# Optimization experiments

Measured on AMD Instinct MI355X. Metric: run time of the kernel, lower is better.

## Reference

```python
import jax, jax.numpy as jnp
import numpy as np

K_SIZE = 3
CH_IN = 256
NFILT = 256

def setup_inputs() -> dict:
    key = jax.random.key(0)
    k1, k2 = jax.random.split(key)
    x = jax.random.normal(k1, (32, 56, 56, CH_IN), dtype=jnp.float32)
    stdv = 1.0 / np.sqrt(K_SIZE * K_SIZE * CH_IN)
    w = jax.random.normal(k2, (K_SIZE, K_SIZE, CH_IN, NFILT), dtype=jnp.float32) * stdv
    pruning_mask = jnp.ones((K_SIZE * K_SIZE * CH_IN, NFILT), dtype=jnp.float32)
    return {"x": x, "w": w, "pruning_mask": pruning_mask}

def _magnitude_aware_weight(w):
    # scale = mean |w| over (kh, kw, cin), per output filter; stop-gradient
    scale = jax.lax.stop_gradient(jnp.mean(jnp.abs(w), axis=(0, 1, 2), keepdims=True))
    bw_no_grad = scale * jnp.sign(w)
    clipped = jnp.clip(w, -1.0, 1.0)
    # STE: forward = scale*sign(w), backward = d(clip(w,-1,1))
    return jax.lax.stop_gradient(bw_no_grad) - jax.lax.stop_gradient(clipped) + clipped

def reference(x, w, pruning_mask):
    kernel = _magnitude_aware_weight(w) * pruning_mask.reshape(K_SIZE, K_SIZE, CH_IN, NFILT)
    out = jax.lax.conv_general_dilated(
        x, kernel,
        window_strides=(1, 1),
        padding="SAME",
        dimension_numbers=("NHWC", "HWIO", "NHWC"),
    )
    return out
```

## Files before the change

### kernel.cpp

```cpp
#include <hip/hip_runtime.h>

typedef unsigned short u16;
typedef u16 u16x8 __attribute__((ext_vector_type(8)));
typedef __bf16 bf16x8 __attribute__((ext_vector_type(8)));
typedef float f32x4 __attribute__((ext_vector_type(4)));

#define NPIX 100352
#define KTOT 2304
#define IMG_PAD (58 * 58 * 256)

static __device__ __forceinline__ u16 f2bf(float f) {
  unsigned u = __float_as_uint(f);
  return (u16)((u + 0x7fffu + ((u >> 16) & 1u)) >> 16);
}

static __device__ __forceinline__ void gld_lds16(const u16* g, u16* l) {
  __builtin_amdgcn_global_load_lds(
      (const __attribute__((address_space(1))) void*)g,
      (__attribute__((address_space(3))) void*)l, 16, 0, 0);
}

static __device__ __forceinline__ int ka_of(int kt) {
  const int khw = kt >> 2;
  const int q = (khw * 11) >> 5;
  const int r = khw - q * 3;
  return (q * 58 + r - 59) * 256 + (kt & 3) * 64;
}

__global__ void scale_accum_k(const float* __restrict__ w, float* __restrict__ scale) {
  const int t = threadIdx.x;
  const float* p = w + (long)blockIdx.x * 64 * 256 + t;
  float acc = 0.f;
#pragma unroll
  for (int e = 0; e < 64; ++e) acc += fabsf(p[(long)e * 256]);
  atomicAdd(&scale[t], acc);
}

__global__ void pack_w_k(const float* __restrict__ w, const float* __restrict__ mask,
                         const float* __restrict__ ssum, u16* __restrict__ wp) {
  __shared__ u16 t[128][33];
  const int k0 = blockIdx.x * 32;
  const int f0 = blockIdx.y * 128;
  const int tid = threadIdx.x;
#pragma unroll
  for (int i = 0; i < 16; ++i) {
    int idx = tid + i * 256;
    int kk = idx >> 7;
    int ff = idx & 127;
    long g = (long)(k0 + kk) * 256 + f0 + ff;
    float wv = w[g];
    float mv = mask[g];
    float sc = ssum[f0 + ff] * (1.0f / 2304.0f);
    float sg = (wv > 0.f) ? 1.f : ((wv < 0.f) ? -1.f : 0.f);
    t[ff][kk] = f2bf(sc * sg * mv);
  }
  __syncthreads();
#pragma unroll
  for (int i = 0; i < 8; ++i) {
    int idx = tid + i * 256;
    int row = idx >> 4;
    int c = idx & 15;
    unsigned v = (unsigned)t[row][2 * c] | ((unsigned)t[row][2 * c + 1] << 16);
    *(unsigned*)(wp + (long)(f0 + row) * KTOT + k0 + 2 * c) = v;
  }
}

__global__ __launch_bounds__(256) void fill_xpad3_k(const float* __restrict__ x,
                                                    u16* __restrict__ xp) {
  const int img = blockIdx.y;
  const int ph = blockIdx.x;
  u16* rowp = xp + ((img * 58 + ph) * 58) * 256;
  const bool irow = (ph >= 1 && ph <= 56);
  const float* xrow = x + ((long)img * 3136 + (ph - 1) * 56) * 256;
  for (int i = threadIdx.x; i < 58 * 32; i += 256) {
    const int pw = i >> 5;
    const int c8 = (i & 31) * 8;
    u16x8 v = {0, 0, 0, 0, 0, 0, 0, 0};
    if (irow && pw >= 1 && pw <= 56) {
      const float* s = xrow + (pw - 1) * 256 + c8;
      float4 a = *(const float4*)s;
      float4 b = *(const float4*)(s + 4);
      v[0] = f2bf(a.x); v[1] = f2bf(a.y); v[2] = f2bf(a.z); v[3] = f2bf(a.w);
      v[4] = f2bf(b.x); v[5] = f2bf(b.y); v[6] = f2bf(b.z); v[7] = f2bf(b.w);
    }
    *(u16x8*)(rowp + pw * 256 + c8) = v;
  }
}

#define STAGE_A8(kt, h, b) do { const int _ka = ka_of(kt); \
    gld_lds16(aptr[(h)*2]     + _ka, As[b] + ldso[(h)*2]); \
    gld_lds16(aptr[(h)*2 + 1] + _ka, As[b] + ldso[(h)*2 + 1]); } while (0)
#define STAGE_B8(kt, h, b) do { const int _kb = (kt) * 64; \
    gld_lds16(bptr[(h)*2]     + _kb, Bs[b] + ldso[(h)*2]); \
    gld_lds16(bptr[(h)*2 + 1] + _kb, Bs[b] + ldso[(h)*2 + 1]); } while (0)

__global__ __launch_bounds__(512, 2) void conv_gemm8_k(
    const u16* __restrict__ xpad, const u16* __restrict__ wp, float* __restrict__ out) {
  __shared__ u16 As[2][256 * 64];
  __shared__ u16 Bs[2][256 * 64];

  const int tid = threadIdx.x;
  const int lane = tid & 63;
  const int wid = tid >> 6;

  const int orig = blockIdx.x;
  const int swz = (orig & 7) * 49 + (orig >> 3);
  const int m0 = swz * 256;

  const int lsub = lane >> 3;
  const int lc = (lane & 7) ^ lsub;
  const u16* aptr[4];
  const u16* bptr[4];
  int ldso[4];
#pragma unroll
  for (int q = 0; q < 4; ++q) {
    const int o = (q >> 1) * 16 + (q & 1) * 8 + wid;
    const int row = o * 8 + lsub;
    const int m = m0 + row;
    const int img = m / 3136, pix = m % 3136;
    aptr[q] = xpad + (long)img * IMG_PAD + ((pix / 56 + 1) * 58 + (pix % 56) + 1) * 256 + lc * 8;
    bptr[q] = wp + (long)row * KTOT + lc * 8;
    ldso[q] = o * 512;
  }

  const int lm = lane & 15, kq = lane >> 4;
  const int wm = wid >> 2, wn = wid & 3;
  int pcq[2];
  pcq[0] = (kq ^ (lm & 7)) * 8;
  pcq[1] = ((4 + kq) ^ (lm & 7)) * 8;
  const int aB = (wm * 128 + lm) * 64;
  const int bB = (wn * 64 + lm) * 64;

  f32x4 acc[8][4] = {};
  bf16x8 bv[4][2];

  STAGE_B8(0, 0, 0); STAGE_B8(0, 1, 0);
  STAGE_A8(0, 0, 0); STAGE_A8(0, 1, 0);
  STAGE_B8(1, 0, 1); STAGE_B8(1, 1, 1);
  asm volatile("s_waitcnt vmcnt(4)" ::: "memory");
  __builtin_amdgcn_s_barrier();
  asm volatile("" ::: "memory");

  for (int J = 0; J < 17; ++J) {
#pragma unroll
    for (int p = 0; p < 8; ++p) {
      const int buf = p >> 2;
      const int pp = p & 3;
      if (pp == 0) {
#pragma unroll
        for (int ni = 0; ni < 4; ++ni)
#pragma unroll
          for (int ct = 0; ct < 2; ++ct)
            bv[ni][ct] = *(const bf16x8*)(Bs[buf] + bB + pcq[ct] + ni * 1024);
      }
      bf16x8 av[2][2];
#pragma unroll
      for (int f = 0; f < 2; ++f)
#pragma unroll
        for (int ct = 0; ct < 2; ++ct)
          av[f][ct] = *(const bf16x8*)(As[buf] + aB + pcq[ct] + pp * 2048 + f * 1024);

      if (p == 0)      STAGE_A8(2 * J + 1, 0, 1);
      else if (p == 1) STAGE_A8(2 * J + 1, 1, 1);
      else if (p == 2) STAGE_B8(2 * J + 2, 0, 0);
      else if (p == 3) { STAGE_B8(2 * J + 2, 1, 0);
                         asm volatile("s_waitcnt vmcnt(4)" ::: "memory"); }
      else if (p == 4) STAGE_A8(2 * J + 2, 0, 0);
      else if (p == 5) STAGE_A8(2 * J + 2, 1, 0);
      else if (p == 6) STAGE_B8(2 * J + 3, 0, 1);
      else             { STAGE_B8(2 * J + 3, 1, 1);
                         asm volatile("s_waitcnt vmcnt(4)" ::: "memory"); }

      __builtin_amdgcn_s_barrier();
      asm volatile("" ::: "memory");
      __builtin_amdgcn_s_setprio(1);
#pragma unroll
      for (int ct = 0; ct < 2; ++ct)
#pragma unroll
        for (int f = 0; f < 2; ++f)
#pragma unroll
          for (int ni = 0; ni < 4; ++ni)
            acc[pp * 2 + f][ni] = __builtin_amdgcn_mfma_f32_16x16x32_bf16(
                av[f][ct], bv[ni][ct], acc[pp * 2 + f][ni], 0, 0, 0);
      __builtin_amdgcn_s_setprio(0);
      asm volatile("" ::: "memory");
      __builtin_amdgcn_s_barrier();
      asm volatile("" ::: "memory");
    }
  }

#pragma unroll
  for (int p = 0; p < 8; ++p) {
    const int buf = p >> 2;
    const int pp = p & 3;
    if (pp == 0) {
#pragma unroll
      for (int ni = 0; ni < 4; ++ni)
#pragma unroll
        for (int ct = 0; ct < 2; ++ct)
          bv[ni][ct] = *(const bf16x8*)(Bs[buf] + bB + pcq[ct] + ni * 1024);
    }
    bf16x8 av[2][2];
#pragma unroll
    for (int f = 0; f < 2; ++f)
#pragma unroll
      for (int ct = 0; ct < 2; ++ct)
        av[f][ct] = *(const bf16x8*)(As[buf] + aB + pcq[ct] + pp * 2048 + f * 1024);

    if (p == 0)      STAGE_A8(35, 0, 1);
    else if (p == 1) STAGE_A8(35, 1, 1);
    else if (p == 3) asm volatile("s_waitcnt vmcnt(0)" ::: "memory");

    __builtin_amdgcn_s_barrier();
    asm volatile("" ::: "memory");
    __builtin_amdgcn_s_setprio(1);
#pragma unroll
    for (int ct = 0; ct < 2; ++ct)
#pragma unroll
      for (int f = 0; f < 2; ++f)
#pragma unroll
        for (int ni = 0; ni < 4; ++ni)
          acc[pp * 2 + f][ni] = __builtin_amdgcn_mfma_f32_16x16x32_bf16(
              av[f][ct], bv[ni][ct], acc[pp * 2 + f][ni], 0, 0, 0);
    __builtin_amdgcn_s_setprio(0);
    asm volatile("" ::: "memory");
    __builtin_amdgcn_s_barrier();
    asm volatile("" ::: "memory");
  }

  float* op = out + (long)(m0 + wm * 128 + kq * 4) * 256 + wn * 64 + lm;
#pragma unroll
  for (int mi = 0; mi < 8; ++mi) {
#pragma unroll
    for (int ni = 0; ni < 4; ++ni) {
      float* p = op + (long)mi * 16 * 256 + ni * 16;
      f32x4 v = acc[mi][ni];
      p[0] = v[0];
      p[256] = v[1];
      p[512] = v[2];
      p[768] = v[3];
    }
  }
}

__global__ __launch_bounds__(256) void conv_gemm_fb_k(
    const float* __restrict__ x, const u16* __restrict__ wp, float* __restrict__ out) {
  __shared__ u16 As[128 * 40];
  __shared__ u16 Bs[128 * 40];
  const int tid = threadIdx.x;
  const int m0 = blockIdx.x * 128;
  const int n0 = blockIdx.y * 128;
  const int cc = tid & 3;
  const int r0 = tid >> 2;
  const int gm0 = m0 + r0;
  const int gm1 = gm0 + 64;
  const int pix0 = gm0 % 3136, oh0 = pix0 / 56, ow0 = pix0 % 56;
  const int pix1 = gm1 % 3136, oh1 = pix1 / 56, ow1 = pix1 % 56;
  const int lane = tid & 63;
  const int wv = tid >> 6;
  const int wm = wv & 1, wn = wv >> 1;
  const int lm = lane & 15, kq = lane >> 4;
  const int aoff = (wm * 64 + lm) * 40 + kq * 8;
  const int boff = (wn * 64 + lm) * 40 + kq * 8;
  u16* as0 = As + r0 * 40 + cc * 8;
  u16* as1 = As + (r0 + 64) * 40 + cc * 8;
  u16* bs0 = Bs + r0 * 40 + cc * 8;
  u16* bs1 = Bs + (r0 + 64) * 40 + cc * 8;
  const u16* wr0 = wp + (long)(n0 + r0) * KTOT + cc * 8;
  const u16* wr1 = wr0 + (long)64 * KTOT;
  f32x4 acc[4][4] = {};
  for (int khw = 0; khw < 9; ++khw) {
    const int dh = khw / 3 - 1;
    const int dw = khw % 3 - 1;
    const bool v0 = ((unsigned)(oh0 + dh) < 56u) && ((unsigned)(ow0 + dw) < 56u);
    const bool v1 = ((unsigned)(oh1 + dh) < 56u) && ((unsigned)(ow1 + dw) < 56u);
    const long p0 = ((long)gm0 + dh * 56 + dw) * 256 + cc * 8;
    const long p1 = ((long)gm1 + dh * 56 + dw) * 256 + cc * 8;
    const u16* wk0 = wr0 + khw * 256;
    const u16* wk1 = wr1 + khw * 256;
    for (int ct = 0; ct < 8; ++ct) {
      const int ci0 = ct * 32;
      u16x8 a0 = {0,0,0,0,0,0,0,0}, a1 = {0,0,0,0,0,0,0,0};
      float4 l0 = make_float4(0,0,0,0), h0 = make_float4(0,0,0,0);
      float4 l1 = make_float4(0,0,0,0), h1 = make_float4(0,0,0,0);
      if (v0) { l0 = *(const float4*)(x + p0 + ci0); h0 = *(const float4*)(x + p0 + ci0 + 4); }
      if (v1) { l1 = *(const float4*)(x + p1 + ci0); h1 = *(const float4*)(x + p1 + ci0 + 4); }
      a0[0]=f2bf(l0.x); a0[1]=f2bf(l0.y); a0[2]=f2bf(l0.z); a0[3]=f2bf(l0.w);
      a0[4]=f2bf(h0.x); a0[5]=f2bf(h0.y); a0[6]=f2bf(h0.z); a0[7]=f2bf(h0.w);
      a1[0]=f2bf(l1.x); a1[1]=f2bf(l1.y); a1[2]=f2bf(l1.z); a1[3]=f2bf(l1.w);
      a1[4]=f2bf(h1.x); a1[5]=f2bf(h1.y); a1[6]=f2bf(h1.z); a1[7]=f2bf(h1.w);
      u16x8 b0 = *(const u16x8*)(wk0 + ci0);
      u16x8 b1 = *(const u16x8*)(wk1 + ci0);
      __syncthreads();
      *(u16x8*)as0 = a0; *(u16x8*)as1 = a1;
      *(u16x8*)bs0 = b0; *(u16x8*)bs1 = b1;
      __syncthreads();
      bf16x8 av[4], bvv[4];
#pragma unroll
      for (int i = 0; i < 4; ++i) av[i] = *(const bf16x8*)(As + aoff + i * 640);
#pragma unroll
      for (int i = 0; i < 4; ++i) bvv[i] = *(const bf16x8*)(Bs + boff + i * 640);
#pragma unroll
      for (int mi = 0; mi < 4; ++mi)
#pragma unroll
        for (int ni = 0; ni < 4; ++ni)
          acc[mi][ni] = __builtin_amdgcn_mfma_f32_16x16x32_bf16(av[mi], bvv[ni], acc[mi][ni], 0, 0, 0);
    }
  }
  float* op = out + (long)(m0 + wm * 64 + kq * 4) * 256 + n0 + wn * 64 + lm;
#pragma unroll
  for (int mi = 0; mi < 4; ++mi)
#pragma unroll
    for (int ni = 0; ni < 4; ++ni) {
      float* p = op + (long)mi * 16 * 256 + ni * 16;
      f32x4 v = acc[mi][ni];
      p[0] = v[0]; p[256] = v[1]; p[512] = v[2]; p[768] = v[3];
    }
}

extern "C" void kernel_launch(void* const* d_in, const int* in_sizes, int n_in,
                              void* d_out, int out_size, void* d_ws, size_t ws_size,
                              hipStream_t stream) {
  const float* x = (const float*)d_in[0];
  const float* w = (const float*)d_in[1];
  const float* mask = (const float*)d_in[2];
  float* out = (float*)d_out;

  float* scale = (float*)d_ws;
  u16* wp = (u16*)((char*)d_ws + 1088);
  u16* xpad = (u16*)((char*)d_ws + 1088 + 1179648);
  const size_t xpad_bytes = (size_t)32 * IMG_PAD * 2;
  const size_t need = 1088 + 1179648 + xpad_bytes;

  hipMemsetAsync(d_ws, 0, 1088, stream);
  scale_accum_k<<<36, 256, 0, stream>>>(w, scale);
  pack_w_k<<<dim3(72, 2), 256, 0, stream>>>(w, mask, scale, wp);
  if (ws_size >= need) {
    fill_xpad3_k<<<dim3(58, 32), 256, 0, stream>>>(x, xpad);
    conv_gemm8_k<<<392, 512, 0, stream>>>(xpad, wp, out);
  } else {
    conv_gemm_fb_k<<<dim3(784, 2), 256, 0, stream>>>(x, wp, out);
  }
}
```

Before: 335.0 us.

## Triple-buffer A tiles and prefetch two k-steps ahead in conv GEMM

The A (im2col input) shared-memory buffer goes from two stages to three, and the loads are rescheduled so A tiles are prefetched two k-steps ahead. B is refilled in place once its fragments are already in registers. The wait threshold rises to vmcnt(8) so more global-to-LDS loads stay in flight, which should hide global memory latency behind the MFMA work. LDS use grows to 160KB per block, which leaves no headroom for a second block and makes the manual buffer rotation and waitcnt bookkeeping more fragile.

```diff
diff --git a/kernel.cpp b/kernel.cpp
--- a/kernel.cpp
+++ b/kernel.cpp
@@ -87,16 +87,47 @@
   }
 }
 
-#define STAGE_A8(kt, h, b) do { const int _ka = ka_of(kt); \
-    gld_lds16(aptr[(h)*2]     + _ka, As[b] + ldso[(h)*2]); \
-    gld_lds16(aptr[(h)*2 + 1] + _ka, As[b] + ldso[(h)*2 + 1]); } while (0)
-#define STAGE_B8(kt, h, b) do { const int _kb = (kt) * 64; \
-    gld_lds16(bptr[(h)*2]     + _kb, Bs[b] + ldso[(h)*2]); \
-    gld_lds16(bptr[(h)*2 + 1] + _kb, Bs[b] + ldso[(h)*2 + 1]); } while (0)
-
-__global__ __launch_bounds__(512, 2) void conv_gemm8_k(
+#define STAGE_A3(kt, h, buf) do { const int _ka = ka_of(kt); \
+    gld_lds16(aptr[(h)*2]     + _ka, (buf) + ldso[(h)*2]); \
+    gld_lds16(aptr[(h)*2 + 1] + _ka, (buf) + ldso[(h)*2 + 1]); } while (0)
+#define STAGE_B3(kt, h, buf) do { const int _kb = (kt) * 64; \
+    gld_lds16(bptr[(h)*2]     + _kb, (buf) + ldso[(h)*2]); \
+    gld_lds16(bptr[(h)*2 + 1] + _kb, (buf) + ldso[(h)*2 + 1]); } while (0)
+#define STAGE_AB3(kt, Aw, Bw) do { STAGE_A3(kt, 1, Aw); STAGE_B3(kt, 0, Bw); } while (0)
+
+#define PHASE(pp, ABUF, BBUF, STAGE_STMT, WAIT_STMT) do {                         \
+    if ((pp) == 0) {                                                              \
+      _Pragma("unroll") for (int ni = 0; ni < 4; ++ni)                            \
+        _Pragma("unroll") for (int ct = 0; ct < 2; ++ct)                          \
+          bv[ni][ct] = *(const bf16x8*)((BBUF) + bB + pcq[ct] + ni * 1024);       \
+    }                                                                             \
+    bf16x8 av[2][2];                                                              \
+    _Pragma("unroll") for (int f = 0; f < 2; ++f)                                 \
+      _Pragma("unroll") for (int ct = 0; ct < 2; ++ct)                            \
+        av[f][ct] = *(const bf16x8*)((ABUF) + aB + pcq[ct] + (pp) * 2048 + f * 1024); \
+    STAGE_STMT;                                                                   \
+    WAIT_STMT;                                                                    \
+    __builtin_amdgcn_s_barrier();                                                 \
+    asm volatile("" ::: "memory");                                                \
+    __builtin_amdgcn_s_setprio(1);                                                \
+    _Pragma("unroll") for (int ct = 0; ct < 2; ++ct)                              \
+      _Pragma("unroll") for (int f = 0; f < 2; ++f)                               \
+        _Pragma("unroll") for (int ni = 0; ni < 4; ++ni)                          \
+          acc[(pp) * 2 + f][ni] = __builtin_amdgcn_mfma_f32_16x16x32_bf16(        \
+              av[f][ct], bv[ni][ct], acc[(pp) * 2 + f][ni], 0, 0, 0);             \
+    __builtin_amdgcn_s_setprio(0);                                                \
+    asm volatile("" ::: "memory");                                                \
+    __builtin_amdgcn_s_barrier();                                                 \
+    asm volatile("" ::: "memory");                                                \
+  } while (0)
+
+#define VMC8 asm volatile("s_waitcnt vmcnt(8)" ::: "memory")
+#define VMC0 asm volatile("s_waitcnt vmcnt(0)" ::: "memory")
+#define NOSTMT do { } while (0)
+
+__global__ __launch_bounds__(512, 2) void conv_gemm9_k(
     const u16* __restrict__ xpad, const u16* __restrict__ wp, float* __restrict__ out) {
-  __shared__ u16 As[2][256 * 64];
+  __shared__ u16 As[3][256 * 64];
   __shared__ u16 Bs[2][256 * 64];
 
   const int tid = threadIdx.x;
@@ -134,98 +165,53 @@
   f32x4 acc[8][4] = {};
   bf16x8 bv[4][2];
 
-  STAGE_B8(0, 0, 0); STAGE_B8(0, 1, 0);
-  STAGE_A8(0, 0, 0); STAGE_A8(0, 1, 0);
-  STAGE_B8(1, 0, 1); STAGE_B8(1, 1, 1);
-  asm volatile("s_waitcnt vmcnt(4)" ::: "memory");
+  STAGE_A3(0, 0, As[0]); STAGE_A3(0, 1, As[0]);
+  STAGE_B3(0, 0, Bs[0]); STAGE_B3(0, 1, Bs[0]);
+  STAGE_A3(1, 0, As[1]); STAGE_A3(1, 1, As[1]);
+  STAGE_B3(1, 0, Bs[1]); STAGE_B3(1, 1, Bs[1]);
+  VMC8;
   __builtin_amdgcn_s_barrier();
   asm volatile("" ::: "memory");
 
-  for (int J = 0; J < 17; ++J) {
-#pragma unroll
-    for (int p = 0; p < 8; ++p) {
-      const int buf = p >> 2;
-      const int pp = p & 3;
-      if (pp == 0) {
-#pragma unroll
-        for (int ni = 0; ni < 4; ++ni)
-#pragma unroll
-          for (int ct = 0; ct < 2; ++ct)
-            bv[ni][ct] = *(const bf16x8*)(Bs[buf] + bB + pcq[ct] + ni * 1024);
-      }
-      bf16x8 av[2][2];
-#pragma unroll
-      for (int f = 0; f < 2; ++f)
-#pragma unroll
-        for (int ct = 0; ct < 2; ++ct)
-          av[f][ct] = *(const bf16x8*)(As[buf] + aB + pcq[ct] + pp * 2048 + f * 1024);
-
-      if (p == 0)      STAGE_A8(2 * J + 1, 0, 1);
-      else if (p == 1) STAGE_A8(2 * J + 1, 1, 1);
-      else if (p == 2) STAGE_B8(2 * J + 2, 0, 0);
-      else if (p == 3) { STAGE_B8(2 * J + 2, 1, 0);
-                         asm volatile("s_waitcnt vmcnt(4)" ::: "memory"); }
-      else if (p == 4) STAGE_A8(2 * J + 2, 0, 0);
-      else if (p == 5) STAGE_A8(2 * J + 2, 1, 0);
-      else if (p == 6) STAGE_B8(2 * J + 3, 0, 1);
-      else             { STAGE_B8(2 * J + 3, 1, 1);
-                         asm volatile("s_waitcnt vmcnt(4)" ::: "memory"); }
-
-      __builtin_amdgcn_s_barrier();
-      asm volatile("" ::: "memory");
-      __builtin_amdgcn_s_setprio(1);
-#pragma unroll
-      for (int ct = 0; ct < 2; ++ct)
-#pragma unroll
-        for (int f = 0; f < 2; ++f)
-#pragma unroll
-          for (int ni = 0; ni < 4; ++ni)
-            acc[pp * 2 + f][ni] = __builtin_amdgcn_mfma_f32_16x16x32_bf16(
-                av[f][ct], bv[ni][ct], acc[pp * 2 + f][ni], 0, 0, 0);
-      __builtin_amdgcn_s_setprio(0);
-      asm volatile("" ::: "memory");
-      __builtin_amdgcn_s_barrier();
-      asm volatile("" ::: "memory");
-    }
-  }
-
-#pragma unroll
-  for (int p = 0; p < 8; ++p) {
-    const int buf = p >> 2;
-    const int pp = p & 3;
-    if (pp == 0) {
-#pragma unroll
-      for (int ni = 0; ni < 4; ++ni)
-#pragma unroll
-        for (int ct = 0; ct < 2; ++ct)
-          bv[ni][ct] = *(const bf16x8*)(Bs[buf] + bB + pcq[ct] + ni * 1024);
-    }
-    bf16x8 av[2][2];
-#pragma unroll
-    for (int f = 0; f < 2; ++f)
-#pragma unroll
-      for (int ct = 0; ct < 2; ++ct)
-        av[f][ct] = *(const bf16x8*)(As[buf] + aB + pcq[ct] + pp * 2048 + f * 1024);
-
-    if (p == 0)      STAGE_A8(35, 0, 1);
-    else if (p == 1) STAGE_A8(35, 1, 1);
-    else if (p == 3) asm volatile("s_waitcnt vmcnt(0)" ::: "memory");
-
-    __builtin_amdgcn_s_barrier();
-    asm volatile("" ::: "memory");
-    __builtin_amdgcn_s_setprio(1);
-#pragma unroll
-    for (int ct = 0; ct < 2; ++ct)
-#pragma unroll
-      for (int f = 0; f < 2; ++f)
-#pragma unroll
-        for (int ni = 0; ni < 4; ++ni)
-          acc[pp * 2 + f][ni] = __builtin_amdgcn_mfma_f32_16x16x32_bf16(
-              av[f][ct], bv[ni][ct], acc[pp * 2 + f][ni], 0, 0, 0);
-    __builtin_amdgcn_s_setprio(0);
-    asm volatile("" ::: "memory");
-    __builtin_amdgcn_s_barrier();
-    asm volatile("" ::: "memory");
+  for (int J6 = 0; J6 < 5; ++J6) {
+    const int kt0 = J6 * 6;
+#pragma unroll
+    for (int u = 0; u < 6; ++u) {
+      const int kt = kt0 + u;
+      u16* Ar = As[u % 3];
+      u16* Br = Bs[u & 1];
+      u16* Aw = As[(u + 2) % 3];
+      u16* Bw = Bs[u & 1];
+      PHASE(0, Ar, Br, STAGE_A3(kt + 2, 0, Aw), NOSTMT);
+      PHASE(1, Ar, Br, STAGE_AB3(kt + 2, Aw, Bw), NOSTMT);
+      PHASE(2, Ar, Br, STAGE_B3(kt + 2, 1, Bw), NOSTMT);
+      PHASE(3, Ar, Br, NOSTMT, VMC8);
+    }
+  }
+
+#pragma unroll
+  for (int u = 0; u < 6; ++u) {
+    const int kt = 30 + u;
+    u16* Ar = As[u % 3];
+    u16* Br = Bs[u & 1];
+    u16* Aw = As[(u + 2) % 3];
+    u16* Bw = Bs[u & 1];
+    if (u < 4) {
+      PHASE(0, Ar, Br, STAGE_A3(kt + 2, 0, Aw), NOSTMT);
+      PHASE(1, Ar, Br, STAGE_AB3(kt + 2, Aw, Bw), NOSTMT);
+      PHASE(2, Ar, Br, STAGE_B3(kt + 2, 1, Bw), NOSTMT);
+      PHASE(3, Ar, Br, NOSTMT, VMC8);
+    } else if (u == 4) {
+      PHASE(0, Ar, Br, NOSTMT, NOSTMT);
+      PHASE(1, Ar, Br, NOSTMT, NOSTMT);
+      PHASE(2, Ar, Br, NOSTMT, NOSTMT);
+      PHASE(3, Ar, Br, NOSTMT, VMC0);
+    } else {
+      PHASE(0, Ar, Br, NOSTMT, NOSTMT);
+      PHASE(1, Ar, Br, NOSTMT, NOSTMT);
+      PHASE(2, Ar, Br, NOSTMT, NOSTMT);
+      PHASE(3, Ar, Br, NOSTMT, NOSTMT);
+    }
   }
 
   float* op = out + (long)(m0 + wm * 128 + kq * 4) * 256 + wn * 64 + lm;
@@ -332,12 +318,12 @@
   const size_t xpad_bytes = (size_t)32 * IMG_PAD * 2;
   const size_t need = 1088 + 1179648 + xpad_bytes;
 
-  hipMemsetAsync(d_ws, 0, 1088, stream);
+  (void)hipMemsetAsync(d_ws, 0, 1088, stream);
   scale_accum_k<<<36, 256, 0, stream>>>(w, scale);
   pack_w_k<<<dim3(72, 2), 256, 0, stream>>>(w, mask, scale, wp);
   if (ws_size >= need) {
     fill_xpad3_k<<<dim3(58, 32), 256, 0, stream>>>(x, xpad);
-    conv_gemm8_k<<<392, 512, 0, stream>>>(xpad, wp, out);
+    conv_gemm9_k<<<392, 512, 0, stream>>>(xpad, wp, out);
   } else {
     conv_gemm_fb_k<<<dim3(784, 2), 256, 0, stream>>>(x, wp, out);
   }
```

After: 344.6 us. 1.03x slower.
